# Optimization experiments

Hardware: AMD Instinct MI355X
Metric: run time of the kernel (lower is better)

Reference implementation:

```python
import jax, jax.numpy as jnp
import numpy as np

D_MODEL = 128
N_HEADS = 4
HEAD_DIM = D_MODEL // N_HEADS


def setup_inputs() -> dict:
    key = jax.random.key(0)
    kx, kq, ko = jax.random.split(key, 3)
    B, T = 4, 4096
    x = jax.random.normal(kx, (B, T, D_MODEL), dtype=jnp.float32)
    s = 1.0 / np.sqrt(D_MODEL)
    # torch nn.Linear weight: [out, in]; y = x @ W.T
    W_qkv = jax.random.uniform(kq, (3 * D_MODEL, D_MODEL), dtype=jnp.float32, minval=-s, maxval=s)
    W_out = jax.random.uniform(ko, (D_MODEL, D_MODEL), dtype=jnp.float32, minval=-s, maxval=s)
    return {"x": x, "W_qkv": W_qkv, "W_out": W_out}


def reference(x, W_qkv, W_out):
    B, T, _ = x.shape
    qkv = (x @ W_qkv.T).reshape(B, T, 3, N_HEADS, HEAD_DIM)
    q, k, v = qkv[:, :, 0], qkv[:, :, 1], qkv[:, :, 2]  # [B,T,H,D]
    # scores: [B,H,T,T]
    scores = jnp.einsum('bthd,bshd->bhts', q, k) / jnp.sqrt(jnp.float32(HEAD_DIM))
    causal = jnp.triu(jnp.ones((T, T), dtype=bool), 1)
    scores = jnp.where(causal, -jnp.inf, scores)
    attn = jax.nn.softmax(scores, axis=-1)
    out = jnp.einsum('bhts,bshd->bthd', attn, v).reshape(B, T, D_MODEL)
    return out @ W_out.T
```

## Files before the change

kernel.cpp:

```cpp
#include <hip/hip_runtime.h>
#include <math.h>

#define B_   4
#define T_   4096
#define DM_  128
#define NH_  4
#define HD_  32
#define TOKENS (B_ * T_)

typedef __attribute__((ext_vector_type(8))) short short8;
typedef __attribute__((ext_vector_type(4))) float floatx4;

__device__ __forceinline__ unsigned short f2bf(float f) {
    union { float f; unsigned int u; } v; v.f = f;
    unsigned int u = v.u;
    u += 0x7fffu + ((u >> 16) & 1u);
    return (unsigned short)(u >> 16);
}
__device__ __forceinline__ void split_bf(float v, unsigned short& hi, unsigned short& lo) {
    unsigned short h = f2bf(v);
    float hf = __uint_as_float(((unsigned int)h) << 16);
    hi = h;
    lo = f2bf(v - hf);
}

#define LROW 136

__global__ __launch_bounds__(256) void qkv_proj_kernel(
    const float* __restrict__ x, const float* __restrict__ Wqkv,
    unsigned short* __restrict__ q_bf, unsigned short* __restrict__ k_bf,
    unsigned short* __restrict__ v_t)
{
    __shared__ __align__(16) unsigned short whi[64 * LROW];
    __shared__ __align__(16) unsigned short wlo[64 * LROW];

    const int tid  = threadIdx.x;
    const int wave = tid >> 6, lane = tid & 63;
    const int m    = lane & 15, q4 = lane >> 4;
    const int m0   = blockIdx.x * 64;
    const int ch   = blockIdx.y;
    const float scale = 0.2550052509571414f;

    {
        const float4* wg = (const float4*)(Wqkv + (size_t)ch * 64 * DM_);
        #pragma unroll
        for (int i = 0; i < 8; ++i) {
            const int f = tid + 256 * i;
            float4 v = wg[f];
            const int row = f >> 5, k4 = f & 31;
            ushort4 h, l;
            split_bf(v.x, h.x, l.x); split_bf(v.y, h.y, l.y);
            split_bf(v.z, h.z, l.z); split_bf(v.w, h.w, l.w);
            *(ushort4*)(whi + row * LROW + k4 * 4) = h;
            *(ushort4*)(wlo + row * LROW + k4 * 4) = l;
        }
    }

    short8 Ah[4], Al[4];
    {
        const float4* xg = (const float4*)(x + (size_t)(m0 + wave * 16 + m) * DM_);
        #pragma unroll
        for (int ks = 0; ks < 4; ++ks) {
            float4 a = xg[ks * 8 + q4 * 2];
            float4 b = xg[ks * 8 + q4 * 2 + 1];
            ushort4 h0, l0, h1, l1;
            split_bf(a.x, h0.x, l0.x); split_bf(a.y, h0.y, l0.y);
            split_bf(a.z, h0.z, l0.z); split_bf(a.w, h0.w, l0.w);
            split_bf(b.x, h1.x, l1.x); split_bf(b.y, h1.y, l1.y);
            split_bf(b.z, h1.z, l1.z); split_bf(b.w, h1.w, l1.w);
            Ah[ks] = short8{(short)h0.x, (short)h0.y, (short)h0.z, (short)h0.w,
                            (short)h1.x, (short)h1.y, (short)h1.z, (short)h1.w};
            Al[ks] = short8{(short)l0.x, (short)l0.y, (short)l0.z, (short)l0.w,
                            (short)l1.x, (short)l1.y, (short)l1.z, (short)l1.w};
        }
    }
    __syncthreads();

    floatx4 acc[4];
    #pragma unroll
    for (int nb = 0; nb < 4; ++nb) {
        floatx4 a = {0.f, 0.f, 0.f, 0.f};
        #pragma unroll
        for (int ks = 0; ks < 4; ++ks) {
            short8 Bh = *(const short8*)(whi + (nb * 16 + m) * LROW + ks * 32 + q4 * 8);
            short8 Bl = *(const short8*)(wlo + (nb * 16 + m) * LROW + ks * 32 + q4 * 8);
            a = __builtin_amdgcn_mfma_f32_16x16x32_bf16(Ah[ks], Bh, a, 0, 0, 0);
            a = __builtin_amdgcn_mfma_f32_16x16x32_bf16(Ah[ks], Bl, a, 0, 0, 0);
            a = __builtin_amdgcn_mfma_f32_16x16x32_bf16(Al[ks], Bh, a, 0, 0, 0);
        }
        acc[nb] = a;
    }
    __syncthreads();

    unsigned short* stage = whi;
    const bool isV = (ch >= 4);
    if (isV) {
        #pragma unroll
        for (int nb = 0; nb < 4; ++nb) {
            ushort4 p;
            p.x = f2bf(acc[nb][0]); p.y = f2bf(acc[nb][1]);
            p.z = f2bf(acc[nb][2]); p.w = f2bf(acc[nb][3]);
            *(ushort4*)(stage + (nb * 16 + m) * 72 + wave * 16 + q4 * 4) = p;
        }
    } else {
        const float scl = (ch < 2) ? scale : 1.0f;
        #pragma unroll
        for (int nb = 0; nb < 4; ++nb)
            #pragma unroll
            for (int reg = 0; reg < 4; ++reg)
                stage[(wave * 16 + q4 * 4 + reg) * 72 + nb * 16 + m]
                    = f2bf(acc[nb][reg] * scl);
    }
    __syncthreads();

    const int b    = m0 >> 12;
    const int t0   = m0 & (T_ - 1);
    const int head = tid >> 7;
    const int hh   = (ch * 2 + head) & 3;
    const int bh   = b * NH_ + hh;
    const int r    = tid & 127;
    if (isV) {
        const int d = r >> 2, qc = r & 3;
        const unsigned short* sp = stage + (head * 32 + d) * 72 + qc * 16;
        short8 v0 = *(const short8*)(sp);
        short8 v1 = *(const short8*)(sp + 8);
        unsigned short* gp = v_t + ((size_t)bh * HD_ + d) * T_ + t0 + qc * 16;
        *(short8*)(gp)     = v0;
        *(short8*)(gp + 8) = v1;
    } else {
        unsigned short* dst = (ch < 2) ? q_bf : k_bf;
        const int t = r >> 1, half = r & 1;
        const unsigned short* sp = stage + t * 72 + head * 32 + half * 16;
        short8 v0 = *(const short8*)(sp);
        short8 v1 = *(const short8*)(sp + 8);
        unsigned short* gp = dst + ((size_t)bh * T_ + t0 + t) * HD_ + half * 16;
        *(short8*)(gp)     = v0;
        *(short8*)(gp + 8) = v1;
    }
}

template<bool LAST>
__device__ __forceinline__ void attn_tile128(
    const char* kLds, const char* vLds, char* pT,
    const int* kOff, const int* pWr, const int* pRd,
    const int* vOffA, const int* vOffB,
    const int m, const int q4, const short8 qf, const short8 ones,
    const int sbN_in, const int limit,
    floatx4& O0, floatx4& O1, float& mx, float& ls)
{
    const int sbN = LAST ? sbN_in : 8;
    const int kN  = sbN >> 1;

    floatx4 st[8];
    #pragma unroll
    for (int sb = 0; sb < 8; ++sb) {
        if (sb >= sbN) continue;
        short8 kfrag = *(const short8*)(kLds + kOff[sb]);
        floatx4 z = {0.f, 0.f, 0.f, 0.f};
        st[sb] = __builtin_amdgcn_mfma_f32_16x16x32_bf16(kfrag, qf, z, 0, 0, 0);
    }

    if (LAST) {
        #pragma unroll
        for (int sb = 0; sb < 8; ++sb) {
            if (sb >= sbN) continue;
            #pragma unroll
            for (int reg = 0; reg < 4; ++reg)
                if (sb * 16 + q4 * 4 + reg > limit) st[sb][reg] = -INFINITY;
        }
    }

    float fm[8];
    #pragma unroll
    for (int sb = 0; sb < 8; ++sb)
        fm[sb] = (sb < sbN) ? fmaxf(fmaxf(st[sb][0], st[sb][1]),
                                    fmaxf(st[sb][2], st[sb][3]))
                            : -INFINITY;
    float rmax = fmaxf(fmaxf(fmaxf(fm[0], fm[1]), fmaxf(fm[2], fm[3])),
                       fmaxf(fmaxf(fm[4], fm[5]), fmaxf(fm[6], fm[7])));
    rmax = fmaxf(rmax, __shfl_xor(rmax, 16, 64));
    rmax = fmaxf(rmax, __shfl_xor(rmax, 32, 64));

    const bool upd = !__all(rmax <= mx);
    if (upd) {
        const float mn = fmaxf(mx, rmax);
        const float alpha = __builtin_amdgcn_exp2f(mx - mn);
        mx = mn;
        #pragma unroll
        for (int reg = 0; reg < 4; ++reg) { O0[reg] *= alpha; O1[reg] *= alpha; }
        ls *= alpha;
    }

    #pragma unroll
    for (int sb = 0; sb < 8; ++sb) {
        if (sb >= sbN) continue;
        float p0 = __builtin_amdgcn_exp2f(st[sb][0] - mx);
        float p1 = __builtin_amdgcn_exp2f(st[sb][1] - mx);
        float p2 = __builtin_amdgcn_exp2f(st[sb][2] - mx);
        float p3 = __builtin_amdgcn_exp2f(st[sb][3] - mx);
        uint2 pk;
        pk.x = __builtin_amdgcn_perm(__float_as_uint(p1), __float_as_uint(p0),
                                     0x07060302);
        pk.y = __builtin_amdgcn_perm(__float_as_uint(p3), __float_as_uint(p2),
                                     0x07060302);
        *(uint2*)(pT + pWr[sb]) = pk;
    }

    __asm__ volatile("s_waitcnt lgkmcnt(0)" ::: "memory");
    __builtin_amdgcn_sched_barrier(0);

    floatx4 ps = {0.f, 0.f, 0.f, 0.f};
    #pragma unroll
    for (int ks = 0; ks < 4; ++ks) {
        if (ks >= kN) continue;
        short8 bfrag = *(const short8*)(pT + pRd[ks]);
        short8 va = *(const short8*)(vLds + vOffA[ks]);
        short8 vb = *(const short8*)(vLds + vOffB[ks]);
        O0 = __builtin_amdgcn_mfma_f32_16x16x32_bf16(va, bfrag, O0, 0, 0, 0);
        O1 = __builtin_amdgcn_mfma_f32_16x16x32_bf16(vb, bfrag, O1, 0, 0, 0);
        ps = __builtin_amdgcn_mfma_f32_16x16x32_bf16(ones, bfrag, ps, 0, 0, 0);
    }
    ls += ps[0];
}

__global__ __launch_bounds__(256, 4) void attn_mfma_kernel(
    const unsigned short* __restrict__ qb, const unsigned short* __restrict__ kb,
    const unsigned short* __restrict__ vtb, float* __restrict__ og)
{
    __shared__ __align__(16) char smem[32768];
    char* kLds = smem;
    char* vLds = smem + 8192;
    const int tid  = threadIdx.x;
    const int wave = tid >> 6, lane = tid & 63;
    const int m    = lane & 15, q4 = lane >> 4;
    char* pT = smem + 16384 + wave * 4096 + m * 256;

    const int pid = blockIdx.x;
    const int xcd = pid & 7;
    const int r_  = pid >> 3;
    const int bh  = xcd * 2 + (r_ & 1);
    const int j_  = r_ >> 1;
    const int a_  = j_ & 15, k_ = j_ >> 4;
    const int qt  = (k_ == 0) ? a_ : (k_ == 1) ? 63 - a_
                  : (k_ == 2) ? 32 + a_ : 31 - a_;

    const size_t qkbase = (size_t)bh * T_ * HD_;
    const char* kg = (const char*)(kb + qkbase);
    const char* vg = (const char*)(vtb + qkbase);

    short8 qf = *(const short8*)((const char*)(qb + qkbase)
                 + (size_t)(qt * 64 + wave * 16 + m) * 64 + q4 * 16);
    const int qrow = wave * 16 + m;

    const short8 ones = short8{(short)0x3F80, (short)0x3F80, (short)0x3F80,
                               (short)0x3F80, (short)0x3F80, (short)0x3F80,
                               (short)0x3F80, (short)0x3F80};

    int kOff[8], pWr[8], pRd[4], vOffA[4], vOffB[4];
    #pragma unroll
    for (int sb = 0; sb < 8; ++sb) {
        kOff[sb] = (sb * 16 + m) * 64 + ((q4 ^ (m & 3)) << 4);
        pWr[sb]  = ((((2 * sb + (q4 >> 1)) ^ m) << 4) + (q4 & 1) * 8);
    }
    #pragma unroll
    for (int ks = 0; ks < 4; ++ks) {
        const int g = ((ks * 4 + q4) ^ m) << 4;
        pRd[ks]   = g;
        vOffA[ks] = m * 256 + g;
        vOffB[ks] = (16 + m) * 256 + g;
    }

    floatx4 O0 = {0.f, 0.f, 0.f, 0.f}, O1 = {0.f, 0.f, 0.f, 0.f};
    float mx = -INFINITY, ls = 0.f;

    const int itN      = (qt >> 1) + 1;
    const int sbN_last = (qt & 1) ? 8 : 4;
    const int limit    = ((qt & 1) << 6) + qrow;

    const int krow = tid >> 2, ku = tid & 3;
    const int vd = tid >> 3, vu = tid & 7;
    const char* kstage = kg + (size_t)krow * 64 + ku * 16;
    const char* vstage = vg + (size_t)vd * (T_ * 2) + vu * 16;

    const int kdst = krow * 64 + ((ku ^ (krow & 3)) << 4);
    const int vdst = vd * 256 + ((vu ^ (vd & 15)) << 4);

    short8 sk0 = *(const short8*)(kstage);
    short8 sk1 = *(const short8*)(kstage + 64 * 64);
    short8 sv0 = *(const short8*)(vstage);
    short8 sv1 = *(const short8*)(vstage + 128);

    for (int it = 0; it < itN; ++it) {
        __syncthreads();
        *(short8*)(kLds + kdst) = sk0;
        *(short8*)(kLds + 64 * 64 + kdst) = sk1;
        *(short8*)(vLds + vdst) = sv0;
        *(short8*)(vLds + (vdst ^ 128)) = sv1;
        __syncthreads();

        if (it + 1 < itN) {
            const size_t nb = (size_t)(it + 1) << 7;
            sk0 = *(const short8*)(kstage + nb * 64);
            sk1 = *(const short8*)(kstage + nb * 64 + 64 * 64);
            sv0 = *(const short8*)(vstage + nb * 2);
            sv1 = *(const short8*)(vstage + nb * 2 + 128);
            attn_tile128<false>(kLds, vLds, pT, kOff, pWr, pRd, vOffA, vOffB,
                                m, q4, qf, ones, 8, 0, O0, O1, mx, ls);
        } else {
            attn_tile128<true>(kLds, vLds, pT, kOff, pWr, pRd, vOffA, vOffB,
                               m, q4, qf, ones, sbN_last, limit,
                               O0, O1, mx, ls);
        }
    }

    const float inv = 1.f / ls;
    const int b = bh >> 2, h = bh & 3;
    const int t = qt * 64 + qrow;
    float* orow = og + (((size_t)b * T_ + t) * NH_ + h) * HD_;
    *(float4*)(orow + q4 * 4)      = make_float4(O0[0] * inv, O0[1] * inv,
                                                 O0[2] * inv, O0[3] * inv);
    *(float4*)(orow + 16 + q4 * 4) = make_float4(O1[0] * inv, O1[1] * inv,
                                                 O1[2] * inv, O1[3] * inv);
}

__global__ __launch_bounds__(256) void out_proj_kernel(
    const float* __restrict__ a, const float* __restrict__ Wout,
    float* __restrict__ out)
{
    __shared__ __align__(16) unsigned short whi[64 * LROW];
    __shared__ __align__(16) unsigned short wlo[64 * LROW];

    const int tid  = threadIdx.x;
    const int wave = tid >> 6, lane = tid & 63;
    const int m    = lane & 15, q4 = lane >> 4;
    const int m0   = blockIdx.x * 64;
    const int ch   = blockIdx.y;

    {
        const float4* wg = (const float4*)(Wout + (size_t)ch * 64 * DM_);
        #pragma unroll
        for (int i = 0; i < 8; ++i) {
            const int f = tid + 256 * i;
            float4 v = wg[f];
            const int row = f >> 5, k4 = f & 31;
            ushort4 h, l;
            split_bf(v.x, h.x, l.x); split_bf(v.y, h.y, l.y);
            split_bf(v.z, h.z, l.z); split_bf(v.w, h.w, l.w);
            *(ushort4*)(whi + row * LROW + k4 * 4) = h;
            *(ushort4*)(wlo + row * LROW + k4 * 4) = l;
        }
    }

    short8 Ah[4], Al[4];
    {
        const float4* xg = (const float4*)(a + (size_t)(m0 + wave * 16 + m) * DM_);
        #pragma unroll
        for (int ks = 0; ks < 4; ++ks) {
            float4 av = xg[ks * 8 + q4 * 2];
            float4 bv = xg[ks * 8 + q4 * 2 + 1];
            ushort4 h0, l0, h1, l1;
            split_bf(av.x, h0.x, l0.x); split_bf(av.y, h0.y, l0.y);
            split_bf(av.z, h0.z, l0.z); split_bf(av.w, h0.w, l0.w);
            split_bf(bv.x, h1.x, l1.x); split_bf(bv.y, h1.y, l1.y);
            split_bf(bv.z, h1.z, l1.z); split_bf(bv.w, h1.w, l1.w);
            Ah[ks] = short8{(short)h0.x, (short)h0.y, (short)h0.z, (short)h0.w,
                            (short)h1.x, (short)h1.y, (short)h1.z, (short)h1.w};
            Al[ks] = short8{(short)l0.x, (short)l0.y, (short)l0.z, (short)l0.w,
                            (short)l1.x, (short)l1.y, (short)l1.z, (short)l1.w};
        }
    }
    __syncthreads();

    #pragma unroll
    for (int nb = 0; nb < 4; ++nb) {
        floatx4 acc = {0.f, 0.f, 0.f, 0.f};
        #pragma unroll
        for (int ks = 0; ks < 4; ++ks) {
            short8 Bh = *(const short8*)(whi + (nb * 16 + m) * LROW + ks * 32 + q4 * 8);
            short8 Bl = *(const short8*)(wlo + (nb * 16 + m) * LROW + ks * 32 + q4 * 8);
            acc = __builtin_amdgcn_mfma_f32_16x16x32_bf16(Ah[ks], Bh, acc, 0, 0, 0);
            acc = __builtin_amdgcn_mfma_f32_16x16x32_bf16(Ah[ks], Bl, acc, 0, 0, 0);
            acc = __builtin_amdgcn_mfma_f32_16x16x32_bf16(Al[ks], Bh, acc, 0, 0, 0);
        }
        const int n = ch * 64 + nb * 16 + m;
        const int tok0 = m0 + wave * 16 + q4 * 4;
        #pragma unroll
        for (int reg = 0; reg < 4; ++reg)
            out[(size_t)(tok0 + reg) * DM_ + n] = acc[reg];
    }
}

extern "C" void kernel_launch(void* const* d_in, const int* in_sizes, int n_in,
                              void* d_out, int out_size, void* d_ws, size_t ws_size,
                              hipStream_t stream) {
    const float* x    = (const float*)d_in[0];
    const float* Wqkv = (const float*)d_in[1];
    const float* Wout = (const float*)d_in[2];
    float* out = (float*)d_out;

    char* ws = (char*)d_ws;
    unsigned short* q_bf  = (unsigned short*)(ws);
    unsigned short* k_bf  = (unsigned short*)(ws + (size_t)4 * 1024 * 1024);
    unsigned short* v_t   = (unsigned short*)(ws + (size_t)8 * 1024 * 1024);
    float*          att_ws = (float*)(ws + (size_t)12 * 1024 * 1024);

    qkv_proj_kernel<<<dim3(TOKENS / 64, 6), 256, 0, stream>>>(x, Wqkv, q_bf, k_bf, v_t);
    attn_mfma_kernel<<<1024, 256, 0, stream>>>(q_bf, k_bf, v_t, att_ws);
    out_proj_kernel<<<dim3(TOKENS / 64, 2), 256, 0, stream>>>(att_ws, Wout, out);
}
```

Measured before the change: 125.9 us.

## Process two query tiles per block to reuse staged K/V tiles

Each attention block now handles 128 query rows (two 64-row groups) instead of 64, so every K/V tile staged into LDS is used by both groups, halving global K/V traffic and staging syncs. The grid shrinks from 1024 to 512 blocks, LDS grows to 48KB for two P buffers per wave, and launch bounds drop to 2 blocks per SM. The cost is fewer blocks, more register and LDS pressure, and possibly lower occupancy and load balance.

```diff
diff --git a/kernel.cpp b/kernel.cpp
--- a/kernel.cpp
+++ b/kernel.cpp
@@ -140,16 +140,14 @@
 }
 
 template<bool LAST>
-__device__ __forceinline__ void attn_tile128(
-    const char* kLds, const char* vLds, char* pT,
-    const int* kOff, const int* pWr, const int* pRd,
-    const int* vOffA, const int* vOffB,
-    const int m, const int q4, const short8 qf, const short8 ones,
+__device__ __forceinline__ void qk_phase(
+    const char* kLds, char* pTg,
+    const int* kOff, const int* pWr,
+    const int q4, const short8 qf,
     const int sbN_in, const int limit,
     floatx4& O0, floatx4& O1, float& mx, float& ls)
 {
     const int sbN = LAST ? sbN_in : 8;
-    const int kN  = sbN >> 1;
 
     floatx4 st[8];
     #pragma unroll
@@ -203,37 +201,22 @@
                                      0x07060302);
         pk.y = __builtin_amdgcn_perm(__float_as_uint(p3), __float_as_uint(p2),
                                      0x07060302);
-        *(uint2*)(pT + pWr[sb]) = pk;
-    }
-
-    __asm__ volatile("s_waitcnt lgkmcnt(0)" ::: "memory");
-    __builtin_amdgcn_sched_barrier(0);
-
-    floatx4 ps = {0.f, 0.f, 0.f, 0.f};
-    #pragma unroll
-    for (int ks = 0; ks < 4; ++ks) {
-        if (ks >= kN) continue;
-        short8 bfrag = *(const short8*)(pT + pRd[ks]);
-        short8 va = *(const short8*)(vLds + vOffA[ks]);
-        short8 vb = *(const short8*)(vLds + vOffB[ks]);
-        O0 = __builtin_amdgcn_mfma_f32_16x16x32_bf16(va, bfrag, O0, 0, 0, 0);
-        O1 = __builtin_amdgcn_mfma_f32_16x16x32_bf16(vb, bfrag, O1, 0, 0, 0);
-        ps = __builtin_amdgcn_mfma_f32_16x16x32_bf16(ones, bfrag, ps, 0, 0, 0);
-    }
-    ls += ps[0];
-}
-
-__global__ __launch_bounds__(256, 4) void attn_mfma_kernel(
+        *(uint2*)(pTg + pWr[sb]) = pk;
+    }
+}
+
+__global__ __launch_bounds__(256, 2) void attn_mfma_kernel(
     const unsigned short* __restrict__ qb, const unsigned short* __restrict__ kb,
     const unsigned short* __restrict__ vtb, float* __restrict__ og)
 {
-    __shared__ __align__(16) char smem[32768];
+    __shared__ __align__(16) char smem[49152];
     char* kLds = smem;
     char* vLds = smem + 8192;
     const int tid  = threadIdx.x;
     const int wave = tid >> 6, lane = tid & 63;
     const int m    = lane & 15, q4 = lane >> 4;
-    char* pT = smem + 16384 + wave * 4096 + m * 256;
+    char* pT0 = smem + 16384 + wave * 8192 + m * 256;
+    char* pT1 = pT0 + 4096;
 
     const int pid = blockIdx.x;
     const int xcd = pid & 7;
@@ -241,15 +224,16 @@
     const int bh  = xcd * 2 + (r_ & 1);
     const int j_  = r_ >> 1;
     const int a_  = j_ & 15, k_ = j_ >> 4;
-    const int qt  = (k_ == 0) ? a_ : (k_ == 1) ? 63 - a_
-                  : (k_ == 2) ? 32 + a_ : 31 - a_;
+    const int p   = (k_ == 0) ? a_ : 31 - a_;
 
     const size_t qkbase = (size_t)bh * T_ * HD_;
     const char* kg = (const char*)(kb + qkbase);
     const char* vg = (const char*)(vtb + qkbase);
 
-    short8 qf = *(const short8*)((const char*)(qb + qkbase)
-                 + (size_t)(qt * 64 + wave * 16 + m) * 64 + q4 * 16);
+    const char* qg = (const char*)(qb + qkbase)
+                   + (size_t)(p * 128 + wave * 16 + m) * 64 + q4 * 16;
+    short8 qf0 = *(const short8*)(qg);
+    short8 qf1 = *(const short8*)(qg + 64 * 64);
     const int qrow = wave * 16 + m;
 
     const short8 ones = short8{(short)0x3F80, (short)0x3F80, (short)0x3F80,
@@ -270,12 +254,11 @@
         vOffB[ks] = (16 + m) * 256 + g;
     }
 
-    floatx4 O0 = {0.f, 0.f, 0.f, 0.f}, O1 = {0.f, 0.f, 0.f, 0.f};
-    float mx = -INFINITY, ls = 0.f;
-
-    const int itN      = (qt >> 1) + 1;
-    const int sbN_last = (qt & 1) ? 8 : 4;
-    const int limit    = ((qt & 1) << 6) + qrow;
+    floatx4 O0g0 = {0.f,0.f,0.f,0.f}, O1g0 = {0.f,0.f,0.f,0.f};
+    floatx4 O0g1 = {0.f,0.f,0.f,0.f}, O1g1 = {0.f,0.f,0.f,0.f};
+    float mx0 = -INFINITY, ls0 = 0.f, mx1 = -INFINITY, ls1 = 0.f;
+
+    const int itN = p + 1;
 
     const int krow = tid >> 2, ku = tid & 3;
     const int vd = tid >> 3, vu = tid & 7;
@@ -298,29 +281,67 @@
         *(short8*)(vLds + (vdst ^ 128)) = sv1;
         __syncthreads();
 
-        if (it + 1 < itN) {
+        const bool last = (it + 1 == itN);
+        if (!last) {
             const size_t nb = (size_t)(it + 1) << 7;
             sk0 = *(const short8*)(kstage + nb * 64);
             sk1 = *(const short8*)(kstage + nb * 64 + 64 * 64);
             sv0 = *(const short8*)(vstage + nb * 2);
             sv1 = *(const short8*)(vstage + nb * 2 + 128);
-            attn_tile128<false>(kLds, vLds, pT, kOff, pWr, pRd, vOffA, vOffB,
-                                m, q4, qf, ones, 8, 0, O0, O1, mx, ls);
+            qk_phase<false>(kLds, pT0, kOff, pWr, q4, qf0, 8, 0,
+                            O0g0, O1g0, mx0, ls0);
+            qk_phase<false>(kLds, pT1, kOff, pWr, q4, qf1, 8, 0,
+                            O0g1, O1g1, mx1, ls1);
         } else {
-            attn_tile128<true>(kLds, vLds, pT, kOff, pWr, pRd, vOffA, vOffB,
-                               m, q4, qf, ones, sbN_last, limit,
-                               O0, O1, mx, ls);
-        }
-    }
-
-    const float inv = 1.f / ls;
+            qk_phase<true>(kLds, pT0, kOff, pWr, q4, qf0, 4, qrow,
+                           O0g0, O1g0, mx0, ls0);
+            qk_phase<true>(kLds, pT1, kOff, pWr, q4, qf1, 8, 64 + qrow,
+                           O0g1, O1g1, mx1, ls1);
+        }
+
+        __asm__ volatile("s_waitcnt lgkmcnt(0)" ::: "memory");
+        __builtin_amdgcn_sched_barrier(0);
+
+        const int kN0 = last ? 2 : 4;
+        floatx4 ps0 = {0.f,0.f,0.f,0.f}, ps1 = {0.f,0.f,0.f,0.f};
+        #pragma unroll
+        for (int ks = 0; ks < 4; ++ks) {
+            short8 va = *(const short8*)(vLds + vOffA[ks]);
+            short8 vb = *(const short8*)(vLds + vOffB[ks]);
+            short8 bf1 = *(const short8*)(pT1 + pRd[ks]);
+            O0g1 = __builtin_amdgcn_mfma_f32_16x16x32_bf16(va, bf1, O0g1, 0, 0, 0);
+            O1g1 = __builtin_amdgcn_mfma_f32_16x16x32_bf16(vb, bf1, O1g1, 0, 0, 0);
+            ps1  = __builtin_amdgcn_mfma_f32_16x16x32_bf16(ones, bf1, ps1, 0, 0, 0);
+            if (ks < kN0) {
+                short8 bf0 = *(const short8*)(pT0 + pRd[ks]);
+                O0g0 = __builtin_amdgcn_mfma_f32_16x16x32_bf16(va, bf0, O0g0, 0, 0, 0);
+                O1g0 = __builtin_amdgcn_mfma_f32_16x16x32_bf16(vb, bf0, O1g0, 0, 0, 0);
+                ps0  = __builtin_amdgcn_mfma_f32_16x16x32_bf16(ones, bf0, ps0, 0, 0, 0);
+            }
+        }
+        ls0 += ps0[0];
+        ls1 += ps1[0];
+    }
+
     const int b = bh >> 2, h = bh & 3;
-    const int t = qt * 64 + qrow;
-    float* orow = og + (((size_t)b * T_ + t) * NH_ + h) * HD_;
-    *(float4*)(orow + q4 * 4)      = make_float4(O0[0] * inv, O0[1] * inv,
-                                                 O0[2] * inv, O0[3] * inv);
-    *(float4*)(orow + 16 + q4 * 4) = make_float4(O1[0] * inv, O1[1] * inv,
-                                                 O1[2] * inv, O1[3] * inv);
+    {
+        const float inv = 1.f / ls0;
+        const int t = p * 128 + qrow;
+        float* orow = og + (((size_t)b * T_ + t) * NH_ + h) * HD_;
+        *(float4*)(orow + q4 * 4)      = make_float4(O0g0[0] * inv, O0g0[1] * inv,
+                                                     O0g0[2] * inv, O0g0[3] * inv);
+        *(float4*)(orow + 16 + q4 * 4) = make_float4(O1g0[0] * inv, O1g0[1] * inv,
+                                                     O1g0[2] * inv, O1g0[3] * inv);
+    }
+    {
+        const float inv = 1.f / ls1;
+        const int t = p * 128 + 64 + qrow;
+        float* orow = og + (((size_t)b * T_ + t) * NH_ + h) * HD_;
+        *(float4*)(orow + q4 * 4)      = make_float4(O0g1[0] * inv, O0g1[1] * inv,
+                                                     O0g1[2] * inv, O0g1[3] * inv);
+        *(float4*)(orow + 16 + q4 * 4) = make_float4(O1g1[0] * inv, O1g1[1] * inv,
+                                                     O1g1[2] * inv, O1g1[3] * inv);
+    }
 }
 
 __global__ __launch_bounds__(256) void out_proj_kernel(
@@ -405,6 +426,6 @@
     float*          att_ws = (float*)(ws + (size_t)12 * 1024 * 1024);
 
     qkv_proj_kernel<<<dim3(TOKENS / 64, 6), 256, 0, stream>>>(x, Wqkv, q_bf, k_bf, v_t);
-    attn_mfma_kernel<<<1024, 256, 0, stream>>>(q_bf, k_bf, v_t, att_ws);
+    attn_mfma_kernel<<<512, 256, 0, stream>>>(q_bf, k_bf, v_t, att_ws);
     out_proj_kernel<<<dim3(TOKENS / 64, 2), 256, 0, stream>>>(att_ws, Wout, out);
 }
```

Measured after the change: 138.6 us. +10.1%, slower.
